# Optimization experiments

Hardware: AMD Instinct MI355X
Metric: run time of the kernel (lower is better)

Reference implementation:

```python
import jax, jax.numpy as jnp
import numpy as np

B, D, OUT, K = 2048, 256, 256, 16


def setup_inputs() -> dict:
    key = jax.random.key(0)
    k1, k2, k3, k4 = jax.random.split(key, 4)
    x = jax.random.normal(k1, (B, D), dtype=jnp.float32)
    values = jax.random.uniform(k2, (OUT, D, K), dtype=jnp.float32, minval=-0.05, maxval=0.05)
    skip_w = jax.random.normal(k3, (OUT, D), dtype=jnp.float32) * (1.0 / np.sqrt(D).astype(np.float32))
    skip_b = jax.random.normal(k4, (OUT,), dtype=jnp.float32) * 0.01
    return {"x": x, "values": values, "skip_w": skip_w, "skip_b": skip_b}


def reference(x, values, skip_w, skip_b):
    # x: (B, D); values: (OUT, D, K); skip_w: (OUT, D); skip_b: (OUT,)
    num_knots = values.shape[-1]
    grid = jnp.linspace(-1.0, 1.0, num_knots)  # (K,)
    xc = jnp.clip(x, -1.0, 1.0)
    # torch.bucketize(x, grid) with right=False == searchsorted side='left'
    right = jnp.searchsorted(grid, xc, side='left')
    left = jnp.clip(right - 1, 0, num_knots - 2)  # (B, D)
    right = left + 1
    g0 = grid[left]
    g1 = grid[right]
    w = (xc - g0) / (g1 - g0 + 1e-12)  # (B, D)
    # Gather spline values per (sample, input-dim) knot bucket.
    vt = jnp.transpose(values, (1, 2, 0))  # (D, K, OUT)
    dim_idx = jnp.arange(xc.shape[1])[None, :]  # (1, D)
    v_left = vt[dim_idx, left]    # (B, D, OUT)
    v_right = vt[dim_idx, right]  # (B, D, OUT)
    # Linear interpolation + sum over input dims.
    y = jnp.sum((1.0 - w)[..., None] * v_left + w[..., None] * v_right, axis=1)  # (B, OUT)
    # Skip connection on the clamped input (torch reassigns x = clamp(x) first).
    return y + xc @ skip_w.T + skip_b
```

## Files before the change

kernel.cpp:

```cpp
#include <hip/hip_runtime.h>
#include <hip/hip_bf16.h>


namespace {
constexpr int Bsz  = 2048;
constexpr int Din  = 256;
constexpr int Dout = 256;
constexpr int Kn   = 16;
constexpr int KKNOT = Din * Kn;
constexpr int Ksp   = KKNOT + Din;
constexpr int KB    = Ksp / 32;
constexpr int KBK   = KKNOT / 32;
constexpr float INV_H = 7.5f;
constexpr float Hgrid = 2.0f / 15.0f;

constexpr int NSPLIT = 9;
constexpr int STK    = 8;
constexpr int STS    = 4;
constexpr int PELEM  = Bsz * Dout;
constexpr int SXS    = 36;
}

typedef __attribute__((ext_vector_type(8))) short shortx8;
typedef __attribute__((ext_vector_type(4))) float floatx4;

__device__ __forceinline__ unsigned int f2bf(float f) {
  __hip_bfloat16 h = __float2bfloat16(f);
  return (unsigned int)*reinterpret_cast<unsigned short*>(&h);
}
__device__ __forceinline__ float clamp1(float v) {
  return fminf(1.f, fmaxf(-1.f, v));
}
__device__ __forceinline__ unsigned int packbf(unsigned int e0, unsigned int e1) {
  return (e1 & 0xffff0000u) | (e0 >> 16);
}
__device__ __forceinline__ unsigned int rnd(float f) {
  return __float_as_uint(f) + 0x8000u;
}

__global__ __launch_bounds__(256) void kan_prep(
    const float* __restrict__ values, const float* __restrict__ skip_w,
    unsigned short* __restrict__ Wf) {
  const int tid = blockIdx.x * 256 + threadIdx.x;
  const int q  = tid & 3;
  const int n  = (tid >> 2) & 15;
  const int og = (tid >> 6) & 15;
  const int kb = tid >> 10;
  const int o  = og * 16 + n;
  const int k0 = kb * 32 + q * 8;
  const float* src = (kb < KBK)
      ? values + (size_t)o * KKNOT + k0
      : skip_w + (size_t)o * Din + (k0 - KKNOT);
  const float4 v0 = *(const float4*)src;
  const float4 v1 = *(const float4*)(src + 4);
  const size_t chunk = (size_t)kb * 1024 + og * 64 + q * 16 + n;
  *(uint4*)(Wf + chunk * 8) = make_uint4(
      f2bf(v0.x) | (f2bf(v0.y) << 16), f2bf(v0.z) | (f2bf(v0.w) << 16),
      f2bf(v1.x) | (f2bf(v1.y) << 16), f2bf(v1.z) | (f2bf(v1.w) << 16));
}

__global__ __launch_bounds__(256) void kan_gemm(
    const float* __restrict__ x, const unsigned short* __restrict__ Wf,
    float* __restrict__ part) {
  __shared__ float sx[32 * SXS];
  __shared__ __align__(16) unsigned short aLds[2][32 * 64];

  const int tid  = threadIdx.x;
  const int wave = tid >> 6, lane = tid & 63;
  const int ks   = blockIdx.x % NSPLIT;
  const int mi   = blockIdx.x / NSPLIT;
  const int m0   = mi * 32;
  const int og0  = wave * 4;
  const int lrow = lane & 15, lq = lane >> 4;

  const int brow = tid >> 3;
  const int bseg = tid & 7;
  const int kbi  = bseg >> 2;
  const int dsel = (bseg >> 1) & 1;
  const float h0 = (float)((bseg & 1) * 8);

  const uint4* B = (const uint4*)Wf;

  floatx4 acc[2][4] = {};
  uint4 bb[2][8];

  if (ks < 8) {
    const int kb0 = ks * 16;
    const int d0  = ks * 32;
    {
      const float4 v = *(const float4*)(x + (size_t)(m0 + brow) * Din + d0 + bseg * 4);
      *(float4*)&sx[brow * SXS + bseg * 4] = v;
    }
    __syncthreads();

    #pragma unroll
    for (int kk = 0; kk < 2; ++kk)
      #pragma unroll
      for (int j = 0; j < 4; ++j)
        bb[0][kk * 4 + j] = B[(size_t)(kb0 + kk) * 1024 + (og0 + j) * 64 + lane];
    {
      const float xv = sx[brow * SXS + 2 * kbi + dsel];
      const float t  = (clamp1(xv) + 1.f) * INV_H;
      unsigned int e[8];
      #pragma unroll
      for (int h = 0; h < 8; ++h)
        e[h] = rnd(fmaxf(0.f, 1.f - fabsf(t - (h0 + (float)h))));
      *(uint4*)&aLds[0][brow * 64 + bseg * 8] =
          make_uint4(packbf(e[0], e[1]), packbf(e[2], e[3]),
                     packbf(e[4], e[5]), packbf(e[6], e[7]));
    }

    for (int s = 0; s < STK; ++s) {
      const int cur = s & 1, nxt = cur ^ 1;
      if (s + 1 < STK) {
        #pragma unroll
        for (int kk = 0; kk < 2; ++kk)
          #pragma unroll
          for (int j = 0; j < 4; ++j)
            bb[nxt][kk * 4 + j] =
                B[(size_t)(kb0 + 2 * (s + 1) + kk) * 1024 + (og0 + j) * 64 + lane];
      }
      __syncthreads();

      if (s + 1 < STK) {
        const float xv = sx[brow * SXS + 4 * (s + 1) + 2 * kbi + dsel];
        const float t  = (clamp1(xv) + 1.f) * INV_H;
        unsigned int e[8];
        #pragma unroll
        for (int h = 0; h < 8; ++h)
          e[h] = rnd(fmaxf(0.f, 1.f - fabsf(t - (h0 + (float)h))));
        *(uint4*)&aLds[nxt][brow * 64 + bseg * 8] =
            make_uint4(packbf(e[0], e[1]), packbf(e[2], e[3]),
                       packbf(e[4], e[5]), packbf(e[6], e[7]));
      }

      shortx8 af[2][2];
      #pragma unroll
      for (int i = 0; i < 2; ++i)
        #pragma unroll
        for (int kk = 0; kk < 2; ++kk)
          af[i][kk] = *(const shortx8*)&aLds[cur][(16 * i + lrow) * 64 + kk * 32 + lq * 8];
      #pragma unroll
      for (int kk = 0; kk < 2; ++kk)
        #pragma unroll
        for (int j = 0; j < 4; ++j) {
          union { uint4 u; shortx8 s; } bc;
          bc.u = bb[cur][kk * 4 + j];
          #pragma unroll
          for (int i = 0; i < 2; ++i)
            acc[i][j] = __builtin_amdgcn_mfma_f32_16x16x32_bf16(af[i][kk], bc.s, acc[i][j], 0, 0, 0);
        }
    }
  } else {
    const int kb0 = KBK;
    const float* xrow = x + (size_t)(m0 + brow) * Din;
    float4 pxa[2], pxb[2];
    #pragma unroll
    for (int kk = 0; kk < 2; ++kk)
      #pragma unroll
      for (int j = 0; j < 4; ++j)
        bb[0][kk * 4 + j] = B[(size_t)(kb0 + kk) * 1024 + (og0 + j) * 64 + lane];
    pxa[0] = *(const float4*)(xrow + bseg * 8);
    pxb[0] = *(const float4*)(xrow + bseg * 8 + 4);
    {
      unsigned int e[8];
      e[0] = rnd(clamp1(pxa[0].x)); e[1] = rnd(clamp1(pxa[0].y));
      e[2] = rnd(clamp1(pxa[0].z)); e[3] = rnd(clamp1(pxa[0].w));
      e[4] = rnd(clamp1(pxb[0].x)); e[5] = rnd(clamp1(pxb[0].y));
      e[6] = rnd(clamp1(pxb[0].z)); e[7] = rnd(clamp1(pxb[0].w));
      *(uint4*)&aLds[0][brow * 64 + bseg * 8] =
          make_uint4(packbf(e[0], e[1]), packbf(e[2], e[3]),
                     packbf(e[4], e[5]), packbf(e[6], e[7]));
    }

    for (int s = 0; s < STS; ++s) {
      const int cur = s & 1, nxt = cur ^ 1;
      if (s + 1 < STS) {
        #pragma unroll
        for (int kk = 0; kk < 2; ++kk)
          #pragma unroll
          for (int j = 0; j < 4; ++j)
            bb[nxt][kk * 4 + j] =
                B[(size_t)(kb0 + 2 * (s + 1) + kk) * 1024 + (og0 + j) * 64 + lane];
        pxa[nxt] = *(const float4*)(xrow + (s + 1) * 64 + bseg * 8);
        pxb[nxt] = *(const float4*)(xrow + (s + 1) * 64 + bseg * 8 + 4);
      }
      __syncthreads();

      if (s + 1 < STS) {
        unsigned int e[8];
        e[0] = rnd(clamp1(pxa[nxt].x)); e[1] = rnd(clamp1(pxa[nxt].y));
        e[2] = rnd(clamp1(pxa[nxt].z)); e[3] = rnd(clamp1(pxa[nxt].w));
        e[4] = rnd(clamp1(pxb[nxt].x)); e[5] = rnd(clamp1(pxb[nxt].y));
        e[6] = rnd(clamp1(pxb[nxt].z)); e[7] = rnd(clamp1(pxb[nxt].w));
        *(uint4*)&aLds[nxt][brow * 64 + bseg * 8] =
            make_uint4(packbf(e[0], e[1]), packbf(e[2], e[3]),
                       packbf(e[4], e[5]), packbf(e[6], e[7]));
      }

      shortx8 af[2][2];
      #pragma unroll
      for (int i = 0; i < 2; ++i)
        #pragma unroll
        for (int kk = 0; kk < 2; ++kk)
          af[i][kk] = *(const shortx8*)&aLds[cur][(16 * i + lrow) * 64 + kk * 32 + lq * 8];
      #pragma unroll
      for (int kk = 0; kk < 2; ++kk)
        #pragma unroll
        for (int j = 0; j < 4; ++j) {
          union { uint4 u; shortx8 s; } bc;
          bc.u = bb[cur][kk * 4 + j];
          #pragma unroll
          for (int i = 0; i < 2; ++i)
            acc[i][j] = __builtin_amdgcn_mfma_f32_16x16x32_bf16(af[i][kk], bc.s, acc[i][j], 0, 0, 0);
        }
    }
  }

  const int wtile = mi * 4 + wave;
  float* P = part + (size_t)ks * PELEM + (size_t)wtile * 2048;
  #pragma unroll
  for (int i = 0; i < 2; ++i)
    #pragma unroll
    for (int j = 0; j < 4; ++j)
      *(floatx4*)&P[((i * 4 + j) * 64 + lane) * 4] = acc[i][j];
}

__global__ __launch_bounds__(256) void kan_reduce(
    const float* __restrict__ part, const float* __restrict__ skip_b,
    float* __restrict__ out) {
  const int tid = blockIdx.x * 256 + threadIdx.x;
  float4 a = make_float4(0.f, 0.f, 0.f, 0.f);
  #pragma unroll
  for (int s = 0; s < NSPLIT; ++s) {
    const float4 p = *(const float4*)(part + (size_t)s * PELEM + (size_t)tid * 4);
    a.x += p.x; a.y += p.y; a.z += p.z; a.w += p.w;
  }
  const int f4    = tid & 511, wtile = tid >> 9;
  const int ij    = f4 >> 6,  lane  = f4 & 63;
  const int i     = ij >> 2,  j     = ij & 3;
  const int mi    = wtile >> 2;
  const int wave  = wtile & 3;
  const int b0    = mi * 32 + 16 * i + (lane >> 4) * 4;
  const int o     = wave * 64 + 16 * j + (lane & 15);
  const float sb  = skip_b[o];
  out[(size_t)(b0 + 0) * Dout + o] = a.x + sb;
  out[(size_t)(b0 + 1) * Dout + o] = a.y + sb;
  out[(size_t)(b0 + 2) * Dout + o] = a.z + sb;
  out[(size_t)(b0 + 3) * Dout + o] = a.w + sb;
}

__device__ __forceinline__ void knot_interp(float xraw, float& xv, float& w, int& l) {
  xv = fminf(1.0f, fmaxf(-1.0f, xraw));
  float t = (xv + 1.0f) * INV_H;
  l = (int)ceilf(t) - 1;
  l = l < 0 ? 0 : (l > Kn - 2 ? Kn - 2 : l);
  float g0 = -1.0f + Hgrid * (float)l;
  w = (xv - g0) * INV_H;
}

__global__ __launch_bounds__(256) void prep_transpose(
    const float* __restrict__ values, const float* __restrict__ skip_w,
    float* __restrict__ vt, float* __restrict__ swt) {
  int idx = blockIdx.x * blockDim.x + threadIdx.x;
  if (idx < Din * Kn * Dout) {
    int k = idx & (Kn - 1);
    int d = (idx >> 4) & (Din - 1);
    int o = idx >> 12;
    vt[(d * Kn + k) * Dout + o] = values[idx];
  }
  if (idx < Dout * Din) {
    int d = idx & (Din - 1);
    int o = idx >> 8;
    swt[d * Dout + o] = skip_w[idx];
  }
}

__global__ __launch_bounds__(256) void kan_main(
    const float* __restrict__ x, const float* __restrict__ vt,
    const float* __restrict__ swt, const float* __restrict__ skip_b,
    float* __restrict__ out) {
  __shared__ float s_w[4][Din];
  __shared__ float s_x[4][Din];
  __shared__ int   s_l[4][Din];
  const int tid = threadIdx.x;
  const int b0  = blockIdx.x * 4;
  for (int i = tid; i < 4 * Din; i += 256) {
    int bb = i >> 8;
    int d  = i & (Din - 1);
    float xv, w; int l;
    knot_interp(x[(b0 + bb) * Din + d], xv, w, l);
    s_w[bb][d] = w; s_x[bb][d] = xv; s_l[bb][d] = l;
  }
  __syncthreads();
  const int g = tid >> 6, lane = tid & 63;
  const int o = lane << 2, b = b0 + g;
  float4 acc = make_float4(0.f, 0.f, 0.f, 0.f);
  for (int d = 0; d < Din; ++d) {
    const float w = s_w[g][d], xv = s_x[g][d];
    const int l = s_l[g][d];
    const float* base = vt + (d * Kn + l) * Dout + o;
    const float4 vl = *(const float4*)(base);
    const float4 vr = *(const float4*)(base + Dout);
    const float4 sw = *(const float4*)(swt + d * Dout + o);
    acc.x = fmaf(xv, sw.x, fmaf(w, vr.x - vl.x, acc.x + vl.x));
    acc.y = fmaf(xv, sw.y, fmaf(w, vr.y - vl.y, acc.y + vl.y));
    acc.z = fmaf(xv, sw.z, fmaf(w, vr.z - vl.z, acc.z + vl.z));
    acc.w = fmaf(xv, sw.w, fmaf(w, vr.w - vl.w, acc.w + vl.w));
  }
  const float4 bias = *(const float4*)(skip_b + o);
  acc.x += bias.x; acc.y += bias.y; acc.z += bias.z; acc.w += bias.w;
  *(float4*)(out + (size_t)b * Dout + o) = acc;
}

extern "C" void kernel_launch(void* const* d_in, const int* in_sizes, int n_in,
                              void* d_out, int out_size, void* d_ws, size_t ws_size,
                              hipStream_t stream) {
  (void)in_sizes; (void)n_in; (void)out_size;
  const float* x      = (const float*)d_in[0];
  const float* values = (const float*)d_in[1];
  const float* skip_w = (const float*)d_in[2];
  const float* skip_b = (const float*)d_in[3];
  float* out = (float*)d_out;

  const size_t wf_bytes   = (size_t)Dout * Ksp * sizeof(unsigned short);
  const size_t part_bytes = (size_t)NSPLIT * PELEM * sizeof(float);
  const size_t need_gemm  = wf_bytes + part_bytes;
  const size_t need_fb    = (size_t)(Din * Kn * Dout + Din * Dout) * sizeof(float);

  if (ws_size >= need_gemm) {
    unsigned short* Wf = (unsigned short*)d_ws;
    float* part = (float*)((char*)d_ws + wf_bytes);
    kan_prep<<<(KB * 1024) / 256, 256, 0, stream>>>(values, skip_w, Wf);
    kan_gemm<<<(Bsz / 32) * NSPLIT, 256, 0, stream>>>(x, Wf, part);
    kan_reduce<<<PELEM / 4 / 256, 256, 0, stream>>>(part, skip_b, out);
  } else if (ws_size >= need_fb) {
    float* vt  = (float*)d_ws;
    float* swt = vt + Din * Kn * Dout;
    prep_transpose<<<(Din * Kn * Dout + 255) / 256, 256, 0, stream>>>(values, skip_w, vt, swt);
    kan_main<<<Bsz / 4, 256, 0, stream>>>(x, vt, swt, skip_b, out);
  }
}
```

Measured before the change: 78.04 us.

## Replace split-K partial buffer and reduce kernel with atomic accumulation into output

The prep kernel now also initializes the output with the skip bias. The GEMM kernel then atomically adds each split-K partial tile directly into the output, so the separate reduce kernel and the 9-way partial buffer go away. This removes one launch and the round trip of 9×2MB of partials through memory, at the cost of scattered scalar float atomics (9-way contention per element) and a summation order that is no longer deterministic.

```diff
diff --git a/kernel.cpp b/kernel.cpp
--- a/kernel.cpp
+++ b/kernel.cpp
@@ -17,7 +17,6 @@
 constexpr int NSPLIT = 9;
 constexpr int STK    = 8;
 constexpr int STS    = 4;
-constexpr int PELEM  = Bsz * Dout;
 constexpr int SXS    = 36;
 }
 
@@ -40,8 +39,14 @@
 
 __global__ __launch_bounds__(256) void kan_prep(
     const float* __restrict__ values, const float* __restrict__ skip_w,
-    unsigned short* __restrict__ Wf) {
+    const float* __restrict__ skip_b, unsigned short* __restrict__ Wf,
+    float* __restrict__ out) {
   const int tid = blockIdx.x * 256 + threadIdx.x;
+  if (tid < Bsz * Dout / 4) {
+    const int base = tid * 4;
+    const float4 b4 = *(const float4*)(skip_b + (base & (Dout - 1)));
+    *(float4*)(out + base) = b4;
+  }
   const int q  = tid & 3;
   const int n  = (tid >> 2) & 15;
   const int og = (tid >> 6) & 15;
@@ -61,7 +66,7 @@
 
 __global__ __launch_bounds__(256) void kan_gemm(
     const float* __restrict__ x, const unsigned short* __restrict__ Wf,
-    float* __restrict__ part) {
+    float* __restrict__ out) {
   __shared__ float sx[32 * SXS];
   __shared__ __align__(16) unsigned short aLds[2][32 * 64];
 
@@ -217,37 +222,17 @@
     }
   }
 
-  const int wtile = mi * 4 + wave;
-  float* P = part + (size_t)ks * PELEM + (size_t)wtile * 2048;
   #pragma unroll
-  for (int i = 0; i < 2; ++i)
+  for (int i = 0; i < 2; ++i) {
+    const int grow = m0 + 16 * i + lq * 4;
     #pragma unroll
-    for (int j = 0; j < 4; ++j)
-      *(floatx4*)&P[((i * 4 + j) * 64 + lane) * 4] = acc[i][j];
-}
-
-__global__ __launch_bounds__(256) void kan_reduce(
-    const float* __restrict__ part, const float* __restrict__ skip_b,
-    float* __restrict__ out) {
-  const int tid = blockIdx.x * 256 + threadIdx.x;
-  float4 a = make_float4(0.f, 0.f, 0.f, 0.f);
-  #pragma unroll
-  for (int s = 0; s < NSPLIT; ++s) {
-    const float4 p = *(const float4*)(part + (size_t)s * PELEM + (size_t)tid * 4);
-    a.x += p.x; a.y += p.y; a.z += p.z; a.w += p.w;
-  }
-  const int f4    = tid & 511, wtile = tid >> 9;
-  const int ij    = f4 >> 6,  lane  = f4 & 63;
-  const int i     = ij >> 2,  j     = ij & 3;
-  const int mi    = wtile >> 2;
-  const int wave  = wtile & 3;
-  const int b0    = mi * 32 + 16 * i + (lane >> 4) * 4;
-  const int o     = wave * 64 + 16 * j + (lane & 15);
-  const float sb  = skip_b[o];
-  out[(size_t)(b0 + 0) * Dout + o] = a.x + sb;
-  out[(size_t)(b0 + 1) * Dout + o] = a.y + sb;
-  out[(size_t)(b0 + 2) * Dout + o] = a.z + sb;
-  out[(size_t)(b0 + 3) * Dout + o] = a.w + sb;
+    for (int j = 0; j < 4; ++j) {
+      const int gcol = wave * 64 + 16 * j + lrow;
+      #pragma unroll
+      for (int r = 0; r < 4; ++r)
+        unsafeAtomicAdd(&out[(size_t)(grow + r) * Dout + gcol], acc[i][j][r]);
+    }
+  }
 }
 
 __device__ __forceinline__ void knot_interp(float xraw, float& xv, float& w, int& l) {
@@ -323,17 +308,13 @@
   const float* skip_b = (const float*)d_in[3];
   float* out = (float*)d_out;
 
-  const size_t wf_bytes   = (size_t)Dout * Ksp * sizeof(unsigned short);
-  const size_t part_bytes = (size_t)NSPLIT * PELEM * sizeof(float);
-  const size_t need_gemm  = wf_bytes + part_bytes;
-  const size_t need_fb    = (size_t)(Din * Kn * Dout + Din * Dout) * sizeof(float);
-
-  if (ws_size >= need_gemm) {
+  const size_t wf_bytes = (size_t)Dout * Ksp * sizeof(unsigned short);
+  const size_t need_fb  = (size_t)(Din * Kn * Dout + Din * Dout) * sizeof(float);
+
+  if (ws_size >= wf_bytes) {
     unsigned short* Wf = (unsigned short*)d_ws;
-    float* part = (float*)((char*)d_ws + wf_bytes);
-    kan_prep<<<(KB * 1024) / 256, 256, 0, stream>>>(values, skip_w, Wf);
-    kan_gemm<<<(Bsz / 32) * NSPLIT, 256, 0, stream>>>(x, Wf, part);
-    kan_reduce<<<PELEM / 4 / 256, 256, 0, stream>>>(part, skip_b, out);
+    kan_prep<<<(KB * 1024) / 256, 256, 0, stream>>>(values, skip_w, skip_b, Wf, out);
+    kan_gemm<<<(Bsz / 32) * NSPLIT, 256, 0, stream>>>(x, Wf, out);
   } else if (ws_size >= need_fb) {
     float* vt  = (float*)d_ws;
     float* swt = vt + Din * Kn * Dout;
```

Result: slower. 84.58 us (+8.4%).

## Fold skip linear term into spline knot weights via hat-basis identity

Applied to the files above, without the earlier changes.

Because the piecewise-linear hat basis reproduces x exactly, the skip term sw·x is absorbed into the knot weights (values + sw·g_k) in the prep kernel. The separate skip K-slice and its GEMM split are removed, so the GEMM does one fewer split and the reduce reads fewer partials. The folded weights are rounded to bf16 together, which slightly changes rounding error.

```diff
diff --git a/kernel.cpp b/kernel.cpp
--- a/kernel.cpp
+++ b/kernel.cpp
@@ -8,15 +8,12 @@
 constexpr int Dout = 256;
 constexpr int Kn   = 16;
 constexpr int KKNOT = Din * Kn;
-constexpr int Ksp   = KKNOT + Din;
-constexpr int KB    = Ksp / 32;
 constexpr int KBK   = KKNOT / 32;
 constexpr float INV_H = 7.5f;
 constexpr float Hgrid = 2.0f / 15.0f;
 
-constexpr int NSPLIT = 9;
+constexpr int NSPLIT = 8;
 constexpr int STK    = 8;
-constexpr int STS    = 4;
 constexpr int PELEM  = Bsz * Dout;
 constexpr int SXS    = 36;
 }
@@ -48,15 +45,24 @@
   const int kb = tid >> 10;
   const int o  = og * 16 + n;
   const int k0 = kb * 32 + q * 8;
-  const float* src = (kb < KBK)
-      ? values + (size_t)o * KKNOT + k0
-      : skip_w + (size_t)o * Din + (k0 - KKNOT);
+  const int d    = k0 >> 4;
+  const int kk0  = k0 & 15;
+  const float sw = skip_w[o * Din + d];
+  const float g0 = -1.f + Hgrid * (float)kk0;
+  const float* src = values + (size_t)o * KKNOT + k0;
   const float4 v0 = *(const float4*)src;
   const float4 v1 = *(const float4*)(src + 4);
+  float e[8];
+  e[0] = v0.x; e[1] = v0.y; e[2] = v0.z; e[3] = v0.w;
+  e[4] = v1.x; e[5] = v1.y; e[6] = v1.z; e[7] = v1.w;
+  unsigned int u[8];
+  #pragma unroll
+  for (int i = 0; i < 8; ++i)
+    u[i] = rnd(fmaf(sw, g0 + Hgrid * (float)i, e[i]));
   const size_t chunk = (size_t)kb * 1024 + og * 64 + q * 16 + n;
   *(uint4*)(Wf + chunk * 8) = make_uint4(
-      f2bf(v0.x) | (f2bf(v0.y) << 16), f2bf(v0.z) | (f2bf(v0.w) << 16),
-      f2bf(v1.x) | (f2bf(v1.y) << 16), f2bf(v1.z) | (f2bf(v1.w) << 16));
+      packbf(u[0], u[1]), packbf(u[2], u[3]),
+      packbf(u[4], u[5]), packbf(u[6], u[7]));
 }
 
 __global__ __launch_bounds__(256) void kan_gemm(
@@ -84,137 +90,71 @@
   floatx4 acc[2][4] = {};
   uint4 bb[2][8];
 
-  if (ks < 8) {
-    const int kb0 = ks * 16;
-    const int d0  = ks * 32;
-    {
-      const float4 v = *(const float4*)(x + (size_t)(m0 + brow) * Din + d0 + bseg * 4);
-      *(float4*)&sx[brow * SXS + bseg * 4] = v;
+  const int kb0 = ks * 16;
+  const int d0  = ks * 32;
+  {
+    const float4 v = *(const float4*)(x + (size_t)(m0 + brow) * Din + d0 + bseg * 4);
+    *(float4*)&sx[brow * SXS + bseg * 4] = v;
+  }
+  __syncthreads();
+
+  #pragma unroll
+  for (int kk = 0; kk < 2; ++kk)
+    #pragma unroll
+    for (int j = 0; j < 4; ++j)
+      bb[0][kk * 4 + j] = B[(size_t)(kb0 + kk) * 1024 + (og0 + j) * 64 + lane];
+  {
+    const float xv = sx[brow * SXS + 2 * kbi + dsel];
+    const float t  = (clamp1(xv) + 1.f) * INV_H;
+    unsigned int e[8];
+    #pragma unroll
+    for (int h = 0; h < 8; ++h)
+      e[h] = rnd(fmaxf(0.f, 1.f - fabsf(t - (h0 + (float)h))));
+    *(uint4*)&aLds[0][brow * 64 + bseg * 8] =
+        make_uint4(packbf(e[0], e[1]), packbf(e[2], e[3]),
+                   packbf(e[4], e[5]), packbf(e[6], e[7]));
+  }
+
+  for (int s = 0; s < STK; ++s) {
+    const int cur = s & 1, nxt = cur ^ 1;
+    if (s + 1 < STK) {
+      #pragma unroll
+      for (int kk = 0; kk < 2; ++kk)
+        #pragma unroll
+        for (int j = 0; j < 4; ++j)
+          bb[nxt][kk * 4 + j] =
+              B[(size_t)(kb0 + 2 * (s + 1) + kk) * 1024 + (og0 + j) * 64 + lane];
     }
     __syncthreads();
 
-    #pragma unroll
-    for (int kk = 0; kk < 2; ++kk)
-      #pragma unroll
-      for (int j = 0; j < 4; ++j)
-        bb[0][kk * 4 + j] = B[(size_t)(kb0 + kk) * 1024 + (og0 + j) * 64 + lane];
-    {
-      const float xv = sx[brow * SXS + 2 * kbi + dsel];
+    if (s + 1 < STK) {
+      const float xv = sx[brow * SXS + 4 * (s + 1) + 2 * kbi + dsel];
       const float t  = (clamp1(xv) + 1.f) * INV_H;
       unsigned int e[8];
       #pragma unroll
       for (int h = 0; h < 8; ++h)
         e[h] = rnd(fmaxf(0.f, 1.f - fabsf(t - (h0 + (float)h))));
-      *(uint4*)&aLds[0][brow * 64 + bseg * 8] =
+      *(uint4*)&aLds[nxt][brow * 64 + bseg * 8] =
           make_uint4(packbf(e[0], e[1]), packbf(e[2], e[3]),
                      packbf(e[4], e[5]), packbf(e[6], e[7]));
     }
 
-    for (int s = 0; s < STK; ++s) {
-      const int cur = s & 1, nxt = cur ^ 1;
-      if (s + 1 < STK) {
+    shortx8 af[2][2];
+    #pragma unroll
+    for (int i = 0; i < 2; ++i)
+      #pragma unroll
+      for (int kk = 0; kk < 2; ++kk)
+        af[i][kk] = *(const shortx8*)&aLds[cur][(16 * i + lrow) * 64 + kk * 32 + lq * 8];
+    #pragma unroll
+    for (int kk = 0; kk < 2; ++kk)
+      #pragma unroll
+      for (int j = 0; j < 4; ++j) {
+        union { uint4 u; shortx8 s; } bc;
+        bc.u = bb[cur][kk * 4 + j];
         #pragma unroll
-        for (int kk = 0; kk < 2; ++kk)
-          #pragma unroll
-          for (int j = 0; j < 4; ++j)
-            bb[nxt][kk * 4 + j] =
-                B[(size_t)(kb0 + 2 * (s + 1) + kk) * 1024 + (og0 + j) * 64 + lane];
+        for (int i = 0; i < 2; ++i)
+          acc[i][j] = __builtin_amdgcn_mfma_f32_16x16x32_bf16(af[i][kk], bc.s, acc[i][j], 0, 0, 0);
       }
-      __syncthreads();
-
-      if (s + 1 < STK) {
-        const float xv = sx[brow * SXS + 4 * (s + 1) + 2 * kbi + dsel];
-        const float t  = (clamp1(xv) + 1.f) * INV_H;
-        unsigned int e[8];
-        #pragma unroll
-        for (int h = 0; h < 8; ++h)
-          e[h] = rnd(fmaxf(0.f, 1.f - fabsf(t - (h0 + (float)h))));
-        *(uint4*)&aLds[nxt][brow * 64 + bseg * 8] =
-            make_uint4(packbf(e[0], e[1]), packbf(e[2], e[3]),
-                       packbf(e[4], e[5]), packbf(e[6], e[7]));
-      }
-
-      shortx8 af[2][2];
-      #pragma unroll
-      for (int i = 0; i < 2; ++i)
-        #pragma unroll
-        for (int kk = 0; kk < 2; ++kk)
-          af[i][kk] = *(const shortx8*)&aLds[cur][(16 * i + lrow) * 64 + kk * 32 + lq * 8];
-      #pragma unroll
-      for (int kk = 0; kk < 2; ++kk)
-        #pragma unroll
-        for (int j = 0; j < 4; ++j) {
-          union { uint4 u; shortx8 s; } bc;
-          bc.u = bb[cur][kk * 4 + j];
-          #pragma unroll
-          for (int i = 0; i < 2; ++i)
-            acc[i][j] = __builtin_amdgcn_mfma_f32_16x16x32_bf16(af[i][kk], bc.s, acc[i][j], 0, 0, 0);
-        }
-    }
-  } else {
-    const int kb0 = KBK;
-    const float* xrow = x + (size_t)(m0 + brow) * Din;
-    float4 pxa[2], pxb[2];
-    #pragma unroll
-    for (int kk = 0; kk < 2; ++kk)
-      #pragma unroll
-      for (int j = 0; j < 4; ++j)
-        bb[0][kk * 4 + j] = B[(size_t)(kb0 + kk) * 1024 + (og0 + j) * 64 + lane];
-    pxa[0] = *(const float4*)(xrow + bseg * 8);
-    pxb[0] = *(const float4*)(xrow + bseg * 8 + 4);
-    {
-      unsigned int e[8];
-      e[0] = rnd(clamp1(pxa[0].x)); e[1] = rnd(clamp1(pxa[0].y));
-      e[2] = rnd(clamp1(pxa[0].z)); e[3] = rnd(clamp1(pxa[0].w));
-      e[4] = rnd(clamp1(pxb[0].x)); e[5] = rnd(clamp1(pxb[0].y));
-      e[6] = rnd(clamp1(pxb[0].z)); e[7] = rnd(clamp1(pxb[0].w));
-      *(uint4*)&aLds[0][brow * 64 + bseg * 8] =
-          make_uint4(packbf(e[0], e[1]), packbf(e[2], e[3]),
-                     packbf(e[4], e[5]), packbf(e[6], e[7]));
-    }
-
-    for (int s = 0; s < STS; ++s) {
-      const int cur = s & 1, nxt = cur ^ 1;
-      if (s + 1 < STS) {
-        #pragma unroll
-        for (int kk = 0; kk < 2; ++kk)
-          #pragma unroll
-          for (int j = 0; j < 4; ++j)
-            bb[nxt][kk * 4 + j] =
-                B[(size_t)(kb0 + 2 * (s + 1) + kk) * 1024 + (og0 + j) * 64 + lane];
-        pxa[nxt] = *(const float4*)(xrow + (s + 1) * 64 + bseg * 8);
-        pxb[nxt] = *(const float4*)(xrow + (s + 1) * 64 + bseg * 8 + 4);
-      }
-      __syncthreads();
-
-      if (s + 1 < STS) {
-        unsigned int e[8];
-        e[0] = rnd(clamp1(pxa[nxt].x)); e[1] = rnd(clamp1(pxa[nxt].y));
-        e[2] = rnd(clamp1(pxa[nxt].z)); e[3] = rnd(clamp1(pxa[nxt].w));
-        e[4] = rnd(clamp1(pxb[nxt].x)); e[5] = rnd(clamp1(pxb[nxt].y));
-        e[6] = rnd(clamp1(pxb[nxt].z)); e[7] = rnd(clamp1(pxb[nxt].w));
-        *(uint4*)&aLds[nxt][brow * 64 + bseg * 8] =
-            make_uint4(packbf(e[0], e[1]), packbf(e[2], e[3]),
-                       packbf(e[4], e[5]), packbf(e[6], e[7]));
-      }
-
-      shortx8 af[2][2];
-      #pragma unroll
-      for (int i = 0; i < 2; ++i)
-        #pragma unroll
-        for (int kk = 0; kk < 2; ++kk)
-          af[i][kk] = *(const shortx8*)&aLds[cur][(16 * i + lrow) * 64 + kk * 32 + lq * 8];
-      #pragma unroll
-      for (int kk = 0; kk < 2; ++kk)
-        #pragma unroll
-        for (int j = 0; j < 4; ++j) {
-          union { uint4 u; shortx8 s; } bc;
-          bc.u = bb[cur][kk * 4 + j];
-          #pragma unroll
-          for (int i = 0; i < 2; ++i)
-            acc[i][j] = __builtin_amdgcn_mfma_f32_16x16x32_bf16(af[i][kk], bc.s, acc[i][j], 0, 0, 0);
-        }
-    }
   }
 
   const int wtile = mi * 4 + wave;
@@ -323,7 +263,7 @@
   const float* skip_b = (const float*)d_in[3];
   float* out = (float*)d_out;
 
-  const size_t wf_bytes   = (size_t)Dout * Ksp * sizeof(unsigned short);
+  const size_t wf_bytes   = (size_t)Dout * KKNOT * sizeof(unsigned short);
   const size_t part_bytes = (size_t)NSPLIT * PELEM * sizeof(float);
   const size_t need_gemm  = wf_bytes + part_bytes;
   const size_t need_fb    = (size_t)(Din * Kn * Dout + Din * Dout) * sizeof(float);
@@ -331,7 +271,7 @@
   if (ws_size >= need_gemm) {
     unsigned short* Wf = (unsigned short*)d_ws;
     float* part = (float*)((char*)d_ws + wf_bytes);
-    kan_prep<<<(KB * 1024) / 256, 256, 0, stream>>>(values, skip_w, Wf);
+    kan_prep<<<(KBK * 1024) / 256, 256, 0, stream>>>(values, skip_w, Wf);
     kan_gemm<<<(Bsz / 32) * NSPLIT, 256, 0, stream>>>(x, Wf, part);
     kan_reduce<<<PELEM / 4 / 256, 256, 0, stream>>>(part, skip_b, out);
   } else if (ws_size >= need_fb) {
```

New measurement: 81.80 us. 1.05x slower.
